# Performance work log

Hardware: AMD Instinct MI355X
Metric: run time of the kernel (lower is better)

## Reference

```python
import jax, jax.numpy as jnp
import numpy as np

B, S, D, H = 2, 2048, 1024, 16
HD = D // H  # 64


def setup_inputs() -> dict:
    key = jax.random.key(0)
    ks = jax.random.split(key, 10)
    inp = {
        "queries": jax.random.normal(ks[0], (B, S, D), dtype=jnp.float32),
        "keys": jax.random.normal(ks[1], (B, S, D), dtype=jnp.float32),
        "values": jax.random.normal(ks[2], (B, S, D), dtype=jnp.float32),
        "attention_mask": jax.random.randint(ks[3], (B, S), 0, 2, dtype=jnp.int32),
        # Linear params (torch nn.Linear: y = x @ W.T + b), scaled like default init
        "Wq": jax.random.normal(ks[4], (D, D), dtype=jnp.float32) / np.sqrt(D),
        "bq": jnp.zeros((D,), dtype=jnp.float32),
        "Wk": jax.random.normal(ks[5], (D, D), dtype=jnp.float32) / np.sqrt(D),
        "bk": jnp.zeros((D,), dtype=jnp.float32),
        "Wv": jax.random.normal(ks[6], (D, D), dtype=jnp.float32) / np.sqrt(D),
        "bv": jnp.zeros((D,), dtype=jnp.float32),
    }
    return inp


def _split_heads(x):
    # torch.chunk along last dim + stack(dim=1) == reshape + transpose
    b, s, d = x.shape
    return x.reshape(b, s, H, HD).transpose(0, 2, 1, 3)  # [B,H,S,hd]


def reference(queries, keys, values, attention_mask, Wq, bq, Wk, bk, Wv, bv):
    q = jax.nn.relu(queries @ Wq.T + bq)
    k = jax.nn.relu(keys @ Wk.T + bk)
    v = jax.nn.relu(values @ Wv.T + bv)
    qh, kh, vh = _split_heads(q), _split_heads(k), _split_heads(v)
    score = jnp.einsum("bhqd,bhkd->bhqk", qh, kh) / jnp.sqrt(jnp.float32(HD))
    # enc mask: [B,1,S,1] broadcast over key dim — masks whole query rows where mask==0
    row_mask = (attention_mask == 0)[:, None, :, None]
    score = jnp.where(row_mask, jnp.float32(-1e9), score)
    attn = jax.nn.softmax(score, axis=-1)
    a = jnp.einsum("bhqk,bhkd->bhqd", attn, vh)  # [B,H,S,hd]
    # faithful to original: permute(0,1,3,2) then reshape to (B,S,D)
    a = a.transpose(0, 1, 3, 2).reshape(q.shape[0], q.shape[1], q.shape[2])
    return a + queries
```

## Files before the change

kernel.cpp:

```cpp
#include <hip/hip_runtime.h>
#include <hip/hip_bf16.h>

#define DEV __device__ __forceinline__

typedef __attribute__((ext_vector_type(8))) short short8;
typedef __attribute__((ext_vector_type(4))) float f32x4;

#define MFMA16(a, b, c) __builtin_amdgcn_mfma_f32_16x16x32_bf16((a), (b), (c), 0, 0, 0)

static constexpr int B_ = 2, S_ = 2048, D_ = 1024, H_ = 16, HD_ = 64;
static constexpr long NX = (long)B_ * S_ * D_;
static constexpr long NW = (long)D_ * D_;

DEV short f2bf(float f) {
    __hip_bfloat16 h = __float2bfloat16(f);
    union { __hip_bfloat16 hh; short s; } u;
    u.hh = h;
    return u.s;
}

DEV float bf2f(short s) {
    union { float f; unsigned u; } x;
    x.u = ((unsigned)(unsigned short)s) << 16;
    return x.f;
}

DEV unsigned pk2(float a, float b) {
    union { float f; unsigned u; } ua, ub;
    ua.f = a; ub.f = b;
    return ((ua.u + 0x8000u) >> 16) | ((ub.u + 0x8000u) & 0xffff0000u);
}

DEV short8 ld8(const short* p) { return *(const short8*)p; }

DEV void gld16(const short* g, short* l) {
    __builtin_amdgcn_global_load_lds(
        (const __attribute__((address_space(1))) unsigned int*)g,
        (__attribute__((address_space(3))) unsigned int*)l, 16, 0, 0);
}

__global__ __launch_bounds__(256) void convert_all(
    const float* __restrict__ q, const float* __restrict__ k, const float* __restrict__ v,
    const float* __restrict__ wq, const float* __restrict__ wk, const float* __restrict__ wv,
    short* __restrict__ qb, short* __restrict__ kb, short* __restrict__ vb,
    short* __restrict__ wqb, short* __restrict__ wkb, short* __restrict__ wvb) {
    long tid = (long)blockIdx.x * 256 + threadIdx.x;
    long e = tid * 4;
    const float* src; short* dst; long off;
    if      (e < NX)            { src = q;  dst = qb;  off = e; }
    else if (e < 2*NX)          { src = k;  dst = kb;  off = e - NX; }
    else if (e < 3*NX)          { src = v;  dst = vb;  off = e - 2*NX; }
    else if (e < 3*NX + NW)     { src = wq; dst = wqb; off = e - 3*NX; }
    else if (e < 3*NX + 2*NW)   { src = wk; dst = wkb; off = e - 3*NX - NW; }
    else                        { src = wv; dst = wvb; off = e - 3*NX - 2*NW; }
    float4 f = *(const float4*)(src + off);
    short4 o;
    o.x = f2bf(f.x); o.y = f2bf(f.y); o.z = f2bf(f.z); o.w = f2bf(f.w);
    *(short4*)(dst + off) = o;
}

__global__ __launch_bounds__(256) void gemm_bias_relu(
    const short* __restrict__ X0, const short* __restrict__ X1, const short* __restrict__ X2,
    const short* __restrict__ W0, const short* __restrict__ W1, const short* __restrict__ W2,
    const float* __restrict__ b0, const float* __restrict__ b1, const float* __restrict__ b2,
    short* __restrict__ O0, short* __restrict__ O1, short* __restrict__ O2) {
    __shared__ short As[2][128 * 32];
    __shared__ short Bs[2][128 * 32];

    const int z = blockIdx.z;
    const short* X   = (z == 0) ? X0 : (z == 1) ? X1 : X2;
    const short* W   = (z == 0) ? W0 : (z == 1) ? W1 : W2;
    const float* bia = (z == 0) ? b0 : (z == 1) ? b1 : b2;
    short*       Out = (z == 0) ? O0 : (z == 1) ? O1 : O2;

    const int tid  = threadIdx.x;
    const int wid  = tid >> 6;
    const int lane = tid & 63;
    const int id   = lane & 15;
    const int quad = lane >> 4;
    const int m0 = blockIdx.y * 128;
    const int n0 = blockIdx.x * 128;
    const int wm = (wid >> 1) * 64;
    const int wn = (wid & 1) * 64;

    const short* Ag0 = X + (long)(m0 + wid * 32 + (lane >> 2)) * D_ + (lane & 3) * 8;
    const short* Bg0 = W + (long)(n0 + wid * 32 + (lane >> 2)) * D_ + (lane & 3) * 8;
    const int offW = wid * 1024;

    f32x4 acc[4][4] = {};

    gld16(Ag0,            &As[0][offW]);
    gld16(Ag0 + 16 * D_,  &As[0][offW + 512]);
    gld16(Bg0,            &Bs[0][offW]);
    gld16(Bg0 + 16 * D_,  &Bs[0][offW + 512]);

    for (int kk = 0; kk < D_; kk += 32) {
        const int cur = (kk >> 5) & 1;
        __syncthreads();
        if (kk + 32 < D_) {
            const int nxt = cur ^ 1;
            gld16(Ag0 + kk + 32,            &As[nxt][offW]);
            gld16(Ag0 + 16 * D_ + kk + 32,  &As[nxt][offW + 512]);
            gld16(Bg0 + kk + 32,            &Bs[nxt][offW]);
            gld16(Bg0 + 16 * D_ + kk + 32,  &Bs[nxt][offW + 512]);
        }

        short8 af[4], bf[4];
#pragma unroll
        for (int i = 0; i < 4; i++) af[i] = ld8(&As[cur][(wm + 16*i + id) * 32 + quad * 8]);
#pragma unroll
        for (int j = 0; j < 4; j++) bf[j] = ld8(&Bs[cur][(wn + 16*j + id) * 32 + quad * 8]);
#pragma unroll
        for (int i = 0; i < 4; i++)
#pragma unroll
            for (int j = 0; j < 4; j++)
                acc[i][j] = MFMA16(af[i], bf[j], acc[i][j]);
    }

#pragma unroll
    for (int j = 0; j < 4; j++) {
        int col = n0 + wn + 16*j + id;
        float bj = bia[col];
#pragma unroll
        for (int i = 0; i < 4; i++) {
#pragma unroll
            for (int r = 0; r < 4; r++) {
                int row = m0 + wm + 16*i + quad*4 + r;
                float val = fmaxf(acc[i][j][r] + bj, 0.f);
                Out[(long)row * D_ + col] = f2bf(val);
            }
        }
    }
}

__global__ __launch_bounds__(256) void transpose_v(const short* __restrict__ Vp,
                                                   short* __restrict__ VT) {
    __shared__ short tile[64 * 64];
    const int bh = blockIdx.y;
    const int b = bh >> 4, h = bh & 15;
    const int s0 = blockIdx.x * 64;
    const int t = threadIdx.x;
#pragma unroll
    for (int it = 0; it < 2; it++) {
        int row = (t >> 3) + 32 * it;
        int u   = t & 7;
        short8 d = ld8(Vp + (long)(b * S_ + s0 + row) * D_ + h * HD_ + u * 8);
        *(short8*)(&tile[row * 64 + (u ^ ((row >> 3) & 7)) * 8]) = d;
    }
    __syncthreads();
#pragma unroll
    for (int it = 0; it < 2; it++) {
        int e  = (t >> 3) + 32 * it;
        int sb = (t & 7) * 8;
        short8 o;
#pragma unroll
        for (int u = 0; u < 8; u++) {
            int row = sb + u;
            o[u] = tile[row * 64 + (((e >> 3) ^ ((row >> 3) & 7)) * 8) + (e & 7)];
        }
        *(short8*)(VT + ((long)bh * HD_ + e) * S_ + s0 + sb) = o;
    }
}

__global__ __launch_bounds__(256, 2) void attention(
    const short* __restrict__ Qb, const short* __restrict__ Kb,
    const short* __restrict__ VT, const int* __restrict__ mask,
    const float* __restrict__ queries, float* __restrict__ out) {
    __shared__ short Ks[2][64 * 64];
    __shared__ short Vs[2][64 * 64];
    __shared__ short pl[4][2 * 16 * 72];

    const int tid  = threadIdx.x;
    const int wid  = tid >> 6;
    const int lane = tid & 63;
    const int id   = lane & 15;
    const int quad = lane >> 4;

    const int bid = blockIdx.x;
    const int w   = bid >> 3;
    const int bh  = (bid & 7) + 8 * (w & 3);
    const int qt  = w >> 2;
    const int b   = bh >> 4;
    const int h   = bh & 15;
    const int q0  = qt * 128 + wid * 32;

    short8 qf[2][2];
#pragma unroll
    for (int g = 0; g < 2; g++) {
        const short* qbase = Qb + (long)(b * S_ + q0 + g * 16 + id) * D_ + h * HD_ + quad * 8;
        short8 f0 = ld8(qbase);
        short8 f1 = ld8(qbase + 32);
        const float qsc = mask[b * S_ + q0 + g * 16 + id] ? 0.125f : 0.f;
#pragma unroll
        for (int i = 0; i < 8; i++) {
            f0[i] = f2bf(bf2f(f0[i]) * qsc);
            f1[i] = f2bf(bf2f(f1[i]) * qsc);
        }
        qf[g][0] = f0; qf[g][1] = f1;
    }

    const int srow = wid * 16 + (lane >> 3);
    const int su   = (lane & 7) ^ (srow & 7);
    const short* kg0 = Kb + ((long)b * S_ + srow) * D_ + h * HD_ + su * 8;
    const short* vg0 = VT + (((long)(b * H_ + h) * HD_) + srow) * S_ + su * 8;
    short* plw = pl[wid];

    const int swz = id & 7;

    float l4[2][4] = {};
    f32x4 o[2][4] = {};

    gld16(kg0,            &Ks[0][wid * 1024]);
    gld16(kg0 + 8 * D_,   &Ks[0][wid * 1024 + 512]);
    gld16(vg0,            &Vs[0][wid * 1024]);
    gld16(vg0 + 8 * S_,   &Vs[0][wid * 1024 + 512]);

    for (int c0 = 0; c0 < S_; c0 += 64) {
        const int cur = (c0 >> 6) & 1;
        __syncthreads();
        if (c0 + 64 < S_) {
            const int nxt = cur ^ 1;
            const long cg = (long)(c0 + 64);
            gld16(kg0 + cg * D_,           &Ks[nxt][wid * 1024]);
            gld16(kg0 + cg * D_ + 8 * D_,  &Ks[nxt][wid * 1024 + 512]);
            gld16(vg0 + cg,                &Vs[nxt][wid * 1024]);
            gld16(vg0 + cg + 8 * S_,       &Vs[nxt][wid * 1024 + 512]);
        }

        f32x4 s[2][4];
#pragma unroll
        for (int g = 0; g < 2; g++)
#pragma unroll
            for (int t = 0; t < 4; t++) s[g][t] = (f32x4){0.f, 0.f, 0.f, 0.f};
#pragma unroll
        for (int t = 0; t < 4; t++) {
            short8 a0 = ld8(&Ks[cur][(16*t + id) * 64 + ((quad    ) ^ swz) * 8]);
            short8 a1 = ld8(&Ks[cur][(16*t + id) * 64 + ((quad ^ 4) ^ swz) * 8]);
            s[0][t] = MFMA16(a0, qf[0][0], s[0][t]);
            s[0][t] = MFMA16(a1, qf[0][1], s[0][t]);
            s[1][t] = MFMA16(a0, qf[1][0], s[1][t]);
            s[1][t] = MFMA16(a1, qf[1][1], s[1][t]);
        }

#pragma unroll
        for (int g = 0; g < 2; g++) {
            short* plg = plw + g * (16 * 72);
#pragma unroll
            for (int t = 0; t < 4; t++) {
                float p0 = __expf(s[g][t][0]);
                float p1 = __expf(s[g][t][1]);
                float p2 = __expf(s[g][t][2]);
                float p3 = __expf(s[g][t][3]);
                l4[g][0] += p0; l4[g][1] += p1; l4[g][2] += p2; l4[g][3] += p3;
                uint2 w2;
                w2.x = pk2(p0, p1);
                w2.y = pk2(p2, p3);
                *(uint2*)(&plg[id * 72 + 16 * t + quad * 4]) = w2;
            }
        }
        short8 pf[2][2];
#pragma unroll
        for (int g = 0; g < 2; g++) {
            short* plg = plw + g * (16 * 72);
            pf[g][0] = ld8(&plg[id * 72 + quad * 8]);
            pf[g][1] = ld8(&plg[id * 72 + 32 + quad * 8]);
        }

#pragma unroll
        for (int j2 = 0; j2 < 4; j2++) {
#pragma unroll
            for (int kh = 0; kh < 2; kh++) {
                short8 va = ld8(&Vs[cur][(16*j2 + id) * 64 + (((kh << 2) + quad) ^ swz) * 8]);
                o[0][j2] = MFMA16(va, pf[0][kh], o[0][j2]);
                o[1][j2] = MFMA16(va, pf[1][kh], o[1][j2]);
            }
        }
    }

    const long obase = (long)b * (S_ * D_) + (long)h * (HD_ * S_);
#pragma unroll
    for (int g = 0; g < 2; g++) {
        float l = l4[g][0] + l4[g][1] + l4[g][2] + l4[g][3];
        l += __shfl_xor(l, 16);
        l += __shfl_xor(l, 32);
        const float linv = 1.f / l;
#pragma unroll
        for (int j2 = 0; j2 < 4; j2++) {
#pragma unroll
            for (int r = 0; r < 4; r++) {
                int dim = 16 * j2 + quad * 4 + r;
                long idx = obase + (long)dim * S_ + q0 + g * 16 + id;
                out[idx] = o[g][j2][r] * linv + queries[idx];
            }
        }
    }
}

extern "C" void kernel_launch(void* const* d_in, const int* in_sizes, int n_in,
                              void* d_out, int out_size, void* d_ws, size_t ws_size,
                              hipStream_t stream) {
    const float* queries = (const float*)d_in[0];
    const float* keys    = (const float*)d_in[1];
    const float* values  = (const float*)d_in[2];
    const int*   mask    = (const int*)d_in[3];
    const float* Wq = (const float*)d_in[4];
    const float* bq = (const float*)d_in[5];
    const float* Wk = (const float*)d_in[6];
    const float* bk = (const float*)d_in[7];
    const float* Wv = (const float*)d_in[8];
    const float* bv = (const float*)d_in[9];
    float* out = (float*)d_out;

    short* ws  = (short*)d_ws;
    short* qb  = ws;
    short* kb  = qb  + NX;
    short* vb  = kb  + NX;
    short* wqb = vb  + NX;
    short* wkb = wqb + NW;
    short* wvb = wkb + NW;
    short* Q   = wvb + NW;
    short* K   = Q   + NX;
    short* Vp  = K   + NX;
    short* VT  = Vp  + NX;

    convert_all<<<15360, 256, 0, stream>>>(queries, keys, values, Wq, Wk, Wv,
                                           qb, kb, vb, wqb, wkb, wvb);
    gemm_bias_relu<<<dim3(8, 32, 3), 256, 0, stream>>>(qb, kb, vb, wqb, wkb, wvb,
                                                       bq, bk, bv, Q, K, Vp);
    transpose_v<<<dim3(32, 32), 256, 0, stream>>>(Vp, VT);
    attention<<<512, 256, 0, stream>>>(Q, K, VT, mask, queries, out);
}
```

Before: 202.7 us.

## Retile QKV GEMM to 256x256 blocks with triple-buffered LDS and swizzle

The QKV projection GEMM moves from 128x128 tiles with 256 threads and double buffering to 256x256 tiles with 512 threads, a 3-stage LDS pipeline with explicit waitcnt/barrier control, an XOR swizzle on LDS columns, and a remapped 1D grid of 192 blocks that spreads tiles across XCDs. Each warp now computes a 128x64 output block. The aim is more data reuse per loaded tile, deeper overlap of loads with MFMA, and fewer LDS bank conflicts. The cost is a much smaller grid, only 192 blocks on a GPU with many CUs, which may leave hardware idle, plus higher register pressure from 32 accumulators per warp.

```diff
diff --git a/kernel.cpp b/kernel.cpp
--- a/kernel.cpp
+++ b/kernel.cpp
@@ -59,15 +59,22 @@
     *(short4*)(dst + off) = o;
 }
 
-__global__ __launch_bounds__(256) void gemm_bias_relu(
+__global__ __launch_bounds__(512, 2) void gemm_bias_relu(
     const short* __restrict__ X0, const short* __restrict__ X1, const short* __restrict__ X2,
     const short* __restrict__ W0, const short* __restrict__ W1, const short* __restrict__ W2,
     const float* __restrict__ b0, const float* __restrict__ b1, const float* __restrict__ b2,
     short* __restrict__ O0, short* __restrict__ O1, short* __restrict__ O2) {
-    __shared__ short As[2][128 * 32];
-    __shared__ short Bs[2][128 * 32];
-
-    const int z = blockIdx.z;
+    constexpr int BK = 32;
+    constexpr int NT = D_ / BK;
+    __shared__ short As[3][256 * BK];
+    __shared__ short Bs[3][256 * BK];
+
+    const int h  = blockIdx.x;
+    const int tl = (h & 7) * 24 + (h >> 3);
+    const int bx = tl & 3;
+    const int by = (tl >> 2) & 15;
+    const int z  = tl >> 6;
+
     const short* X   = (z == 0) ? X0 : (z == 1) ? X1 : X2;
     const short* W   = (z == 0) ? W0 : (z == 1) ? W1 : W2;
     const float* bia = (z == 0) ? b0 : (z == 1) ? b1 : b2;
@@ -78,56 +85,80 @@
     const int lane = tid & 63;
     const int id   = lane & 15;
     const int quad = lane >> 4;
-    const int m0 = blockIdx.y * 128;
-    const int n0 = blockIdx.x * 128;
-    const int wm = (wid >> 1) * 64;
-    const int wn = (wid & 1) * 64;
-
-    const short* Ag0 = X + (long)(m0 + wid * 32 + (lane >> 2)) * D_ + (lane & 3) * 8;
-    const short* Bg0 = W + (long)(n0 + wid * 32 + (lane >> 2)) * D_ + (lane & 3) * 8;
-    const int offW = wid * 1024;
-
-    f32x4 acc[4][4] = {};
-
-    gld16(Ag0,            &As[0][offW]);
-    gld16(Ag0 + 16 * D_,  &As[0][offW + 512]);
-    gld16(Bg0,            &Bs[0][offW]);
-    gld16(Bg0 + 16 * D_,  &Bs[0][offW + 512]);
-
-    for (int kk = 0; kk < D_; kk += 32) {
-        const int cur = (kk >> 5) & 1;
-        __syncthreads();
-        if (kk + 32 < D_) {
-            const int nxt = cur ^ 1;
-            gld16(Ag0 + kk + 32,            &As[nxt][offW]);
-            gld16(Ag0 + 16 * D_ + kk + 32,  &As[nxt][offW + 512]);
-            gld16(Bg0 + kk + 32,            &Bs[nxt][offW]);
-            gld16(Bg0 + 16 * D_ + kk + 32,  &Bs[nxt][offW + 512]);
-        }
-
-        short8 af[4], bf[4];
-#pragma unroll
-        for (int i = 0; i < 4; i++) af[i] = ld8(&As[cur][(wm + 16*i + id) * 32 + quad * 8]);
-#pragma unroll
-        for (int j = 0; j < 4; j++) bf[j] = ld8(&Bs[cur][(wn + 16*j + id) * 32 + quad * 8]);
-#pragma unroll
-        for (int i = 0; i < 4; i++)
+    const int m0 = by * 256;
+    const int n0 = bx * 256;
+    const int wmo = (wid >> 2) * 128;
+    const int wno = (wid & 3) * 64;
+
+    const int r0 = tid >> 2;
+    const int su = ((tid & 3) ^ (r0 & 3)) * 8;
+    const short* Ag0 = X + (long)(m0 + r0) * D_ + su;
+    const short* Ag1 = Ag0 + (long)128 * D_;
+    const short* Bg0 = W + (long)(n0 + r0) * D_ + su;
+    const short* Bg1 = Bg0 + (long)128 * D_;
+    const int ldst = wid * 512;
+
+    f32x4 acc[8][4] = {};
+
+#define STAGE(t, buf)                                   \
+    do {                                                \
+        const int kk_ = (t) * BK;                       \
+        gld16(Ag0 + kk_, &As[(buf)][ldst]);             \
+        gld16(Ag1 + kk_, &As[(buf)][4096 + ldst]);      \
+        gld16(Bg0 + kk_, &Bs[(buf)][ldst]);             \
+        gld16(Bg1 + kk_, &Bs[(buf)][4096 + ldst]);      \
+    } while (0)
+
+    STAGE(0, 0);
+    STAGE(1, 1);
+    asm volatile("s_waitcnt vmcnt(4)" ::: "memory");
+    __builtin_amdgcn_s_barrier();
+    __builtin_amdgcn_sched_barrier(0);
+
+    const int ksw = (quad ^ (id & 3)) * 8;
+    int cur = 0;
+    for (int t = 0; t < NT; ++t) {
+        int pre = cur + 2; if (pre >= 3) pre -= 3;
+        if (t + 2 < NT) STAGE(t + 2, pre);
+
+        short8 af[8], bf[4];
+#pragma unroll
+        for (int i = 0; i < 8; i++)
+            af[i] = ld8(&As[cur][(wmo + 16 * i + id) * 32 + ksw]);
+#pragma unroll
+        for (int j = 0; j < 4; j++)
+            bf[j] = ld8(&Bs[cur][(wno + 16 * j + id) * 32 + ksw]);
+
+        __builtin_amdgcn_s_setprio(1);
+#pragma unroll
+        for (int i = 0; i < 8; i++)
 #pragma unroll
             for (int j = 0; j < 4; j++)
                 acc[i][j] = MFMA16(af[i], bf[j], acc[i][j]);
-    }
+        __builtin_amdgcn_s_setprio(0);
+
+        if (t + 1 < NT) {
+            if (t + 2 < NT)
+                asm volatile("s_waitcnt vmcnt(4) lgkmcnt(0)" ::: "memory");
+            else
+                asm volatile("s_waitcnt vmcnt(0) lgkmcnt(0)" ::: "memory");
+            __builtin_amdgcn_s_barrier();
+            __builtin_amdgcn_sched_barrier(0);
+        }
+        cur = (cur == 2) ? 0 : cur + 1;
+    }
+#undef STAGE
 
 #pragma unroll
     for (int j = 0; j < 4; j++) {
-        int col = n0 + wn + 16*j + id;
-        float bj = bia[col];
-#pragma unroll
-        for (int i = 0; i < 4; i++) {
+        const int col = n0 + wno + 16 * j + id;
+        const float bj = bia[col];
+#pragma unroll
+        for (int i = 0; i < 8; i++) {
 #pragma unroll
             for (int r = 0; r < 4; r++) {
-                int row = m0 + wm + 16*i + quad*4 + r;
-                float val = fmaxf(acc[i][j][r] + bj, 0.f);
-                Out[(long)row * D_ + col] = f2bf(val);
+                const int row = m0 + wmo + 16 * i + quad * 4 + r;
+                Out[(long)row * D_ + col] = f2bf(fmaxf(acc[i][j][r] + bj, 0.f));
             }
         }
     }
@@ -325,8 +356,8 @@
 
     convert_all<<<15360, 256, 0, stream>>>(queries, keys, values, Wq, Wk, Wv,
                                            qb, kb, vb, wqb, wkb, wvb);
-    gemm_bias_relu<<<dim3(8, 32, 3), 256, 0, stream>>>(qb, kb, vb, wqb, wkb, wvb,
-                                                       bq, bk, bv, Q, K, Vp);
+    gemm_bias_relu<<<dim3(192, 1, 1), 512, 0, stream>>>(qb, kb, vb, wqb, wkb, wvb,
+                                                        bq, bk, bv, Q, K, Vp);
     transpose_v<<<dim3(32, 32), 256, 0, stream>>>(Vp, VT);
     attention<<<512, 256, 0, stream>>>(Q, K, VT, mask, queries, out);
 }
```

After: 214.1 us. 5.7% more time.
